# Optimization experiments

Measured on AMD Instinct MI355X. Metric: run time of the kernel, lower is better.

Reference implementation:

```python
import jax, jax.numpy as jnp
import numpy as np

B, C, D, H, W = 4, 128, 16, 16, 16
CQ = C // 8

def setup_inputs() -> dict:
    key = jax.random.key(0)
    ks = jax.random.split(key, 8)
    s = 0.05
    return {
        "x": jax.random.normal(ks[0], (B, C, D, H, W), dtype=jnp.float32),
        "wq": jax.random.normal(ks[1], (CQ, C), dtype=jnp.float32) * s,
        "bq": jax.random.normal(ks[2], (CQ,), dtype=jnp.float32) * s,
        "wk": jax.random.normal(ks[3], (CQ, C), dtype=jnp.float32) * s,
        "bk": jax.random.normal(ks[4], (CQ,), dtype=jnp.float32) * s,
        "wv": jax.random.normal(ks[5], (C, C), dtype=jnp.float32) * s,
        "bv": jax.random.normal(ks[6], (C,), dtype=jnp.float32) * s,
        "gamma": jax.random.normal(ks[7], (1,), dtype=jnp.float32),
    }

def reference(x, wq, bq, wk, bk, wv, bv, gamma):
    b, c, d, h, w = x.shape
    n = d * h * w
    xf = x.reshape(b, c, n)                                  # [B,C,N]
    # 1x1x1 convs == channel-wise linear projections
    q = jnp.einsum('bcn,qc->bqn', xf, wq) + bq[None, :, None]  # [B,CQ,N]
    k = jnp.einsum('bcn,qc->bqn', xf, wk) + bk[None, :, None]  # [B,CQ,N]
    v = jnp.einsum('bcn,oc->bon', xf, wv) + bv[None, :, None]  # [B,C,N]
    # energy[b,i,j] = sum_c q[b,c,i] * k[b,c,j]  (query permuted to [B,N,CQ])
    energy = jnp.einsum('bci,bcj->bij', q, k)                # [B,N,N]
    attn = jax.nn.softmax(energy, axis=-1)                   # [B,N,N]
    # out = bmm(value, attn^T): out[b,c,i] = sum_j v[b,c,j] * attn[b,i,j]
    out = jnp.einsum('bcj,bij->bci', v, attn)                # [B,C,N]
    out = out.reshape(b, c, d, h, w)
    return gamma[0] * out + x
```

## Files before the change

kernel.cpp:

```cpp
#include <hip/hip_runtime.h>
#include <stdint.h>

#define NT 4096
#define L2E 1.44269504f

typedef short s16x8 __attribute__((ext_vector_type(8)));
typedef short s16x4 __attribute__((ext_vector_type(4)));
typedef float f32x16 __attribute__((ext_vector_type(16)));
typedef float f32x4 __attribute__((ext_vector_type(4)));

__device__ __forceinline__ unsigned short f2bf(float f) {
  unsigned int u = __float_as_uint(f);
  u = u + 0x7FFFu + ((u >> 16) & 1u);
  return (unsigned short)(u >> 16);
}

__device__ __forceinline__ void pack_pa(const float* p, s16x8* pa) {
  unsigned w8[8];
#pragma unroll
  for (int m = 0; m < 8; ++m)
    asm("v_cvt_pk_bf16_f32 %0, %1, %2" : "=v"(w8[m]) : "v"(p[2 * m]), "v"(p[2 * m + 1]));
  unsigned a0 = w8[0], b0 = w8[2]; asm("v_permlane32_swap_b32 %0, %1" : "+v"(a0), "+v"(b0));
  unsigned a1 = w8[1], b1 = w8[3]; asm("v_permlane32_swap_b32 %0, %1" : "+v"(a1), "+v"(b1));
  unsigned c0 = w8[4], d0 = w8[6]; asm("v_permlane32_swap_b32 %0, %1" : "+v"(c0), "+v"(d0));
  unsigned c1 = w8[5], d1 = w8[7]; asm("v_permlane32_swap_b32 %0, %1" : "+v"(c1), "+v"(d1));
  union PW { unsigned u[4]; s16x8 v; } q0, q1;
  q0.u[0] = a0; q0.u[1] = a1; q0.u[2] = b0; q0.u[3] = b1;
  q1.u[0] = c0; q1.u[1] = c1; q1.u[2] = d0; q1.u[3] = d1;
  pa[0] = q0.v; pa[1] = q1.v;
}

__device__ __forceinline__ void merge_write(float* scr, const f32x16 (&acc)[4],
                                            int lc, int hi) {
#pragma unroll
  for (int cb = 0; cb < 4; ++cb)
#pragma unroll
    for (int r = 0; r < 16; ++r) {
      int i = (r & 3) + 8 * (r >> 2) + 4 * hi;
      scr[i * 132 + cb * 32 + lc] = acc[cb][r];
    }
}
__device__ __forceinline__ void merge_add(const float* scr, f32x16 (&acc)[4],
                                          int lc, int hi) {
#pragma unroll
  for (int cb = 0; cb < 4; ++cb)
#pragma unroll
    for (int r = 0; r < 16; ++r) {
      int i = (r & 3) + 8 * (r >> 2) + 4 * hi;
      acc[cb][r] += scr[i * 132 + cb * 32 + lc];
    }
}

__global__ __launch_bounds__(512, 2) void proj_kern(
    const float* __restrict__ x,
    const float* __restrict__ wq, const float* __restrict__ bq,
    const float* __restrict__ wk, const float* __restrict__ bk,
    const float* __restrict__ wv, const float* __restrict__ bv,
    short* __restrict__ qws, short* __restrict__ kws, short* __restrict__ vfrag) {
  __shared__ __align__(16) unsigned short w_s[160 * 128];
  __shared__ __align__(16) unsigned short xv_s[128 * 72];

  int t = threadIdx.x;
  int blk = blockIdx.x;
  int b = blk >> 6;
  int n0 = (blk & 63) * 64;

  for (int i4 = t; i4 < 5120; i4 += 512) {
    int row = i4 >> 5, ka = (i4 & 31) * 4;
    f32x4 v;
    float sc = 1.0f;
    if (row < 128)      v = *(const f32x4*)(wv + row * 128 + ka);
    else if (row < 144) v = *(const f32x4*)(wq + (row - 128) * 128 + ka);
    else              { v = *(const f32x4*)(wk + (row - 144) * 128 + ka); sc = L2E; }
    s16x4 o;
#pragma unroll
    for (int j = 0; j < 4; ++j) o[j] = (short)f2bf(v[j] * sc);
    unsigned byt = ((unsigned)(ka * 2)) ^ (((unsigned)row & 7u) << 4);
    *(s16x4*)((char*)w_s + row * 256 + byt) = o;
  }
  {
    int cL = t >> 4, nn4 = (t & 15) * 4;
    for (int cc = 0; cc < 128; cc += 32) {
      int c = cc + cL;
      f32x4 v = *(const f32x4*)(x + ((size_t)b * 128 + c) * NT + n0 + nn4);
      s16x4 o;
#pragma unroll
      for (int j = 0; j < 4; ++j) o[j] = (short)f2bf(v[j]);
      *(s16x4*)(xv_s + c * 64 + nn4) = o;
    }
  }
  __syncthreads();

  int w = t >> 6, lane = t & 63, lc = lane & 31, hi = lane >> 5;
  int rblk = w >> 1, nc = w & 1;
  int nn = nc * 32 + lc;

  f32x16 zf = {0.f,0.f,0.f,0.f,0.f,0.f,0.f,0.f,0.f,0.f,0.f,0.f,0.f,0.f,0.f,0.f};
  f32x16 acc = zf, acc2 = zf;

#pragma unroll
  for (int kk = 0; kk < 8; ++kk) {
    int kb0 = kk * 16 + hi * 8;
    s16x8 xf;
#pragma unroll
    for (int e = 0; e < 8; ++e) xf[e] = (short)xv_s[(kb0 + e) * 64 + nn];
    unsigned byt = ((unsigned)(kk * 32 + hi * 16)) ^ (((unsigned)lc & 7u) << 4);
    s16x8 af = *(const s16x8*)((const char*)w_s + (rblk * 32 + lc) * 256 + byt);
    acc = __builtin_amdgcn_mfma_f32_32x32x16_bf16(af, xf, acc, 0, 0, 0);
    if (rblk == 3) {
      s16x8 af2 = *(const s16x8*)((const char*)w_s + (128 + lc) * 256 + byt);
      acc2 = __builtin_amdgcn_mfma_f32_32x32x16_bf16(af2, xf, acc2, 0, 0, 0);
    }
  }

  if (rblk == 3) {
    size_t nidx = ((size_t)b * NT + n0 + nn) * 16;
    s16x4 q0, q1, k0, k1;
#pragma unroll
    for (int j = 0; j < 4; ++j) {
      q0[j] = (short)f2bf(acc2[j]      + bq[j + 4 * hi]);
      q1[j] = (short)f2bf(acc2[j + 4]  + bq[j + 8 + 4 * hi]);
      k0[j] = (short)f2bf(acc2[j + 8]  + bk[j + 4 * hi] * L2E);
      k1[j] = (short)f2bf(acc2[j + 12] + bk[j + 8 + 4 * hi] * L2E);
    }
    *(s16x4*)(qws + nidx + 4 * hi)     = q0;
    *(s16x4*)(qws + nidx + 8 + 4 * hi) = q1;
    *(s16x4*)(kws + nidx + 4 * hi)     = k0;
    *(s16x4*)(kws + nidx + 8 + 4 * hi) = k1;
  }

  __syncthreads();
#pragma unroll
  for (int r = 0; r < 16; ++r) {
    int c = rblk * 32 + (r & 3) + 8 * (r >> 2) + 4 * hi;
    xv_s[c * 72 + nn] = f2bf(acc[r] + bv[c]);
  }
  __syncthreads();
#pragma unroll
  for (int p = 0; p < 2; ++p) {
    int gid = t + p * 512;
    int c = gid & 127, ng = gid >> 7;
    s16x8 v = *(const s16x8*)(xv_s + c * 72 + ng * 8);
    size_t idx = (((size_t)b * 256 + (n0 >> 4) + (ng >> 1)) * 128 + c) * 16 + (ng & 1) * 8;
    *(s16x8*)(vfrag + idx) = v;
  }
}

__global__ __launch_bounds__(256, 4) void attn_mfma(
    const short* __restrict__ qws, const short* __restrict__ kws, const short* __restrict__ vfrag,
    const float* __restrict__ x, const float* __restrict__ gp, float* __restrict__ out) {
  __shared__ __align__(16) unsigned char lds[34432];

  int g = blockIdx.x;
  int gg = (g & 7) * 64 + (g >> 3);
  int b = gg >> 7;
  int it = gg & 127;
  int t = threadIdx.x;
  int w = t >> 6, lane = t & 63, lc = lane & 31, hi = lane >> 5;
  int jt0 = w * 1024;

  const short* qb = qws + (size_t)b * NT * 16;
  const short* kb = kws + (size_t)b * NT * 16;
  const short* vfb = vfrag + (size_t)b * 256 * 128 * 16;

  s16x8 qf = *(const s16x8*)(qb + (size_t)(it * 32 + lc) * 16 + hi * 8);

  f32x16 zf = {0.f,0.f,0.f,0.f,0.f,0.f,0.f,0.f,0.f,0.f,0.f,0.f,0.f,0.f,0.f,0.f};
  f32x16 acc[4];
#pragma unroll
  for (int j = 0; j < 4; ++j) acc[j] = zf;
  float lsum = 0.f;

  for (int st = 0; st < 32; ++st) {
    int j0 = jt0 + st * 32;
    int jtb = j0 >> 4;
    s16x8 kf = *(const s16x8*)(kb + (size_t)(j0 + lc) * 16 + hi * 8);
    s16x8 v0[4];
#pragma unroll
    for (int cb = 0; cb < 4; ++cb)
      v0[cb] = *(const s16x8*)(vfb + ((size_t)jtb * 128 + cb * 32 + lc) * 16 + hi * 8);

    f32x16 e = __builtin_amdgcn_mfma_f32_32x32x16_bf16(kf, qf, zf, 0, 0, 0);
#pragma unroll
    for (int r = 0; r < 16; ++r) e[r] = __builtin_amdgcn_exp2f(e[r]);
    float a0 = 0.f;
#pragma unroll
    for (int r = 0; r < 16; ++r) a0 += e[r];
    lsum += a0;

    s16x8 pa[2];
    pack_pa((const float*)&e, pa);

    __builtin_amdgcn_s_setprio(1);
#pragma unroll
    for (int cb = 0; cb < 4; ++cb)
      acc[cb] = __builtin_amdgcn_mfma_f32_32x32x16_bf16(pa[0], v0[cb], acc[cb], 0, 0, 0);
    __builtin_amdgcn_s_setprio(0);

    s16x8 v1[4];
#pragma unroll
    for (int cb = 0; cb < 4; ++cb)
      v1[cb] = *(const s16x8*)(vfb + ((size_t)(jtb + 1) * 128 + cb * 32 + lc) * 16 + hi * 8);

    __builtin_amdgcn_s_setprio(1);
#pragma unroll
    for (int cb = 0; cb < 4; ++cb)
      acc[cb] = __builtin_amdgcn_mfma_f32_32x32x16_bf16(pa[1], v1[cb], acc[cb], 0, 0, 0);
    __builtin_amdgcn_s_setprio(0);
  }

  float* rg0  = (float*)lds;
  float* rg1  = (float*)(lds + 16896);
  float* lsc  = (float*)(lds + 33792);
  float* linv = (float*)(lds + 34304);

  float lf = lsum + __shfl_xor(lsum, 32);
  if (hi == 0) lsc[w * 32 + lc] = lf;
  if (w == 2) merge_write(rg0, acc, lc, hi);
  if (w == 3) merge_write(rg1, acc, lc, hi);
  __syncthreads();
  if (t < 32) {
    float L = lsc[t] + lsc[32 + t] + lsc[64 + t] + lsc[96 + t];
    linv[t] = 1.0f / L;
  }
  if (w == 0) merge_add(rg0, acc, lc, hi);
  if (w == 1) merge_add(rg1, acc, lc, hi);
  __syncthreads();
  if (w == 1) merge_write(rg0, acc, lc, hi);
  __syncthreads();
  if (w == 0) {
    merge_add(rg0, acc, lc, hi);
    merge_write(rg0, acc, lc, hi);
  }
  __syncthreads();

  float gam = gp[0];
  int cc = t >> 1, ih = (t & 1) * 16;
  const float* xb = x + ((size_t)b * 128 + cc) * NT + it * 32 + ih;
  float* ob = out + ((size_t)b * 128 + cc) * NT + it * 32 + ih;
#pragma unroll
  for (int q2 = 0; q2 < 4; ++q2) {
    f32x4 xv = *(const f32x4*)(xb + q2 * 4);
    f32x4 ov;
#pragma unroll
    for (int j = 0; j < 4; ++j) {
      int i = ih + q2 * 4 + j;
      ov[j] = gam * rg0[i * 132 + cc] * linv[i] + xv[j];
    }
    *(f32x4*)(ob + q2 * 4) = ov;
  }
}

extern "C" void kernel_launch(void* const* d_in, const int* in_sizes, int n_in,
                              void* d_out, int out_size, void* d_ws, size_t ws_size,
                              hipStream_t stream) {
  const float* x     = (const float*)d_in[0];
  const float* wq    = (const float*)d_in[1];
  const float* bq    = (const float*)d_in[2];
  const float* wk    = (const float*)d_in[3];
  const float* bk    = (const float*)d_in[4];
  const float* wv    = (const float*)d_in[5];
  const float* bv    = (const float*)d_in[6];
  const float* gamma = (const float*)d_in[7];
  float* out = (float*)d_out;

  short* qws   = (short*)d_ws;
  short* kws   = qws + (size_t)4 * NT * 16;
  short* vfrag = kws + (size_t)4 * NT * 16;

  proj_kern<<<256, 512, 0, stream>>>(x, wq, bq, wk, bk, wv, bv, qws, kws, vfrag);
  attn_mfma<<<512, 256, 0, stream>>>(qws, kws, vfrag, x, gamma, out);
}
```

Baseline: 45.05 us.

## Split attention keys across two blocks and merge partials in a separate kernel

Splits the key dimension into two halves, so the attention kernel runs 1024 blocks instead of 512. Each block writes unnormalized partial outputs and row sums to workspace, and a new merge kernel combines them, normalizes, and adds the residual. The inner loop is also software-pipelined: the next QK MFMA and the K fragment two steps ahead are issued during the current step's exp and PV work. This trades extra global traffic (about 16 MB of partials written and read) and one more launch for better occupancy and latency hiding.

```diff
diff --git a/kernel.cpp b/kernel.cpp
--- a/kernel.cpp
+++ b/kernel.cpp
@@ -146,18 +146,19 @@
   }
 }
 
-__global__ __launch_bounds__(256, 4) void attn_mfma(
+__global__ __launch_bounds__(256) void attn_part(
     const short* __restrict__ qws, const short* __restrict__ kws, const short* __restrict__ vfrag,
-    const float* __restrict__ x, const float* __restrict__ gp, float* __restrict__ out) {
+    float* __restrict__ Dp, float* __restrict__ Lp) {
   __shared__ __align__(16) unsigned char lds[34432];
 
   int g = blockIdx.x;
-  int gg = (g & 7) * 64 + (g >> 3);
-  int b = gg >> 7;
-  int it = gg & 127;
+  int gg = (g & 7) * 128 + (g >> 3);
+  int b = gg >> 8;
+  int it = (gg >> 1) & 127;
+  int js = gg & 1;
   int t = threadIdx.x;
   int w = t >> 6, lane = t & 63, lc = lane & 31, hi = lane >> 5;
-  int jt0 = w * 1024;
+  int jt0 = js * 2048 + w * 512;
 
   const short* qb = qws + (size_t)b * NT * 16;
   const short* kb = kws + (size_t)b * NT * 16;
@@ -171,48 +172,52 @@
   for (int j = 0; j < 4; ++j) acc[j] = zf;
   float lsum = 0.f;
 
-  for (int st = 0; st < 32; ++st) {
-    int j0 = jt0 + st * 32;
-    int jtb = j0 >> 4;
-    s16x8 kf = *(const s16x8*)(kb + (size_t)(j0 + lc) * 16 + hi * 8);
-    s16x8 v0[4];
+  s16x8 kfA = *(const s16x8*)(kb + (size_t)(jt0 + lc) * 16 + hi * 8);
+  f32x16 eA = __builtin_amdgcn_mfma_f32_32x32x16_bf16(kfA, qf, zf, 0, 0, 0);
+  s16x8 kfB = *(const s16x8*)(kb + (size_t)(jt0 + 32 + lc) * 16 + hi * 8);
+  f32x16 eB = zf;
+
+  auto body = [&](int st, f32x16& eCur, f32x16& eNxt, s16x8& kfNxt, s16x8& kfFar) {
+    int jtb = (jt0 >> 4) + st * 2;
+    s16x8 vc[2][4];
+#pragma unroll
+    for (int sl = 0; sl < 2; ++sl)
+#pragma unroll
+      for (int cb = 0; cb < 4; ++cb)
+        vc[sl][cb] = *(const s16x8*)(vfb + ((size_t)(jtb + sl) * 128 + cb * 32 + lc) * 16 + hi * 8);
+
+#pragma unroll
+    for (int r = 0; r < 16; ++r) eCur[r] = __builtin_amdgcn_exp2f(eCur[r]);
+    float a0 = 0.f;
+#pragma unroll
+    for (int r = 0; r < 16; ++r) a0 += eCur[r];
+    lsum += a0;
+    s16x8 pa[2];
+    pack_pa((const float*)&eCur, pa);
+
+    if (st < 15)
+      eNxt = __builtin_amdgcn_mfma_f32_32x32x16_bf16(kfNxt, qf, zf, 0, 0, 0);
+    if (st < 14)
+      kfFar = *(const s16x8*)(kb + (size_t)(jt0 + (st + 2) * 32 + lc) * 16 + hi * 8);
+
+    __builtin_amdgcn_s_setprio(1);
 #pragma unroll
     for (int cb = 0; cb < 4; ++cb)
-      v0[cb] = *(const s16x8*)(vfb + ((size_t)jtb * 128 + cb * 32 + lc) * 16 + hi * 8);
-
-    f32x16 e = __builtin_amdgcn_mfma_f32_32x32x16_bf16(kf, qf, zf, 0, 0, 0);
-#pragma unroll
-    for (int r = 0; r < 16; ++r) e[r] = __builtin_amdgcn_exp2f(e[r]);
-    float a0 = 0.f;
-#pragma unroll
-    for (int r = 0; r < 16; ++r) a0 += e[r];
-    lsum += a0;
-
-    s16x8 pa[2];
-    pack_pa((const float*)&e, pa);
-
-    __builtin_amdgcn_s_setprio(1);
+      acc[cb] = __builtin_amdgcn_mfma_f32_32x32x16_bf16(pa[0], vc[0][cb], acc[cb], 0, 0, 0);
 #pragma unroll
     for (int cb = 0; cb < 4; ++cb)
-      acc[cb] = __builtin_amdgcn_mfma_f32_32x32x16_bf16(pa[0], v0[cb], acc[cb], 0, 0, 0);
+      acc[cb] = __builtin_amdgcn_mfma_f32_32x32x16_bf16(pa[1], vc[1][cb], acc[cb], 0, 0, 0);
     __builtin_amdgcn_s_setprio(0);
-
-    s16x8 v1[4];
-#pragma unroll
-    for (int cb = 0; cb < 4; ++cb)
-      v1[cb] = *(const s16x8*)(vfb + ((size_t)(jtb + 1) * 128 + cb * 32 + lc) * 16 + hi * 8);
-
-    __builtin_amdgcn_s_setprio(1);
-#pragma unroll
-    for (int cb = 0; cb < 4; ++cb)
-      acc[cb] = __builtin_amdgcn_mfma_f32_32x32x16_bf16(pa[1], v1[cb], acc[cb], 0, 0, 0);
-    __builtin_amdgcn_s_setprio(0);
-  }
-
-  float* rg0  = (float*)lds;
-  float* rg1  = (float*)(lds + 16896);
-  float* lsc  = (float*)(lds + 33792);
-  float* linv = (float*)(lds + 34304);
+  };
+
+  for (int sp = 0; sp < 8; ++sp) {
+    body(2 * sp,     eA, eB, kfB, kfA);
+    body(2 * sp + 1, eB, eA, kfA, kfB);
+  }
+
+  float* rg0 = (float*)lds;
+  float* rg1 = (float*)(lds + 16896);
+  float* lsc = (float*)(lds + 33792);
 
   float lf = lsum + __shfl_xor(lsum, 32);
   if (hi == 0) lsc[w * 32 + lc] = lf;
@@ -221,34 +226,46 @@
   __syncthreads();
   if (t < 32) {
     float L = lsc[t] + lsc[32 + t] + lsc[64 + t] + lsc[96 + t];
-    linv[t] = 1.0f / L;
+    Lp[((size_t)js * 4 + b) * NT + it * 32 + t] = L;
   }
   if (w == 0) merge_add(rg0, acc, lc, hi);
   if (w == 1) merge_add(rg1, acc, lc, hi);
   __syncthreads();
   if (w == 1) merge_write(rg0, acc, lc, hi);
   __syncthreads();
-  if (w == 0) {
-    merge_add(rg0, acc, lc, hi);
-    merge_write(rg0, acc, lc, hi);
-  }
-  __syncthreads();
-
+  if (w == 0) { merge_add(rg0, acc, lc, hi); merge_write(rg0, acc, lc, hi); }
+  __syncthreads();
+
+  int cc = t >> 1, ih = (t & 1) * 16;
+  float* dp = Dp + (((size_t)js * 4 + b) * 128 + cc) * NT + it * 32 + ih;
+#pragma unroll
+  for (int q2 = 0; q2 < 4; ++q2) {
+    f32x4 ov;
+#pragma unroll
+    for (int j = 0; j < 4; ++j) ov[j] = rg0[(ih + q2 * 4 + j) * 132 + cc];
+    *(f32x4*)(dp + q2 * 4) = ov;
+  }
+}
+
+__global__ __launch_bounds__(256) void merge_kern(
+    const float* __restrict__ Dp, const float* __restrict__ Lp,
+    const float* __restrict__ x, const float* __restrict__ gp,
+    float* __restrict__ out) {
+  int idx = blockIdx.x * 256 + threadIdx.x;
+  size_t off = (size_t)idx * 4;
+  int n = (int)(off & (NT - 1));
+  int b = (int)(off >> 19);
   float gam = gp[0];
-  int cc = t >> 1, ih = (t & 1) * 16;
-  const float* xb = x + ((size_t)b * 128 + cc) * NT + it * 32 + ih;
-  float* ob = out + ((size_t)b * 128 + cc) * NT + it * 32 + ih;
-#pragma unroll
-  for (int q2 = 0; q2 < 4; ++q2) {
-    f32x4 xv = *(const f32x4*)(xb + q2 * 4);
-    f32x4 ov;
-#pragma unroll
-    for (int j = 0; j < 4; ++j) {
-      int i = ih + q2 * 4 + j;
-      ov[j] = gam * rg0[i * 132 + cc] * linv[i] + xv[j];
-    }
-    *(f32x4*)(ob + q2 * 4) = ov;
-  }
+  f32x4 d0 = *(const f32x4*)(Dp + off);
+  f32x4 d1 = *(const f32x4*)(Dp + (size_t)4 * 128 * NT + off);
+  f32x4 l0 = *(const f32x4*)(Lp + (size_t)b * NT + n);
+  f32x4 l1 = *(const f32x4*)(Lp + (size_t)4 * NT + (size_t)b * NT + n);
+  f32x4 xv = *(const f32x4*)(x + off);
+  f32x4 ov;
+#pragma unroll
+  for (int j = 0; j < 4; ++j)
+    ov[j] = gam * (d0[j] + d1[j]) / (l0[j] + l1[j]) + xv[j];
+  *(f32x4*)(out + off) = ov;
 }
 
 extern "C" void kernel_launch(void* const* d_in, const int* in_sizes, int n_in,
@@ -267,7 +284,10 @@
   short* qws   = (short*)d_ws;
   short* kws   = qws + (size_t)4 * NT * 16;
   short* vfrag = kws + (size_t)4 * NT * 16;
+  float* Dp    = (float*)(vfrag + (size_t)4 * 256 * 128 * 16);
+  float* Lp    = Dp + (size_t)2 * 4 * 128 * NT;
 
   proj_kern<<<256, 512, 0, stream>>>(x, wq, bq, wk, bk, wv, bv, qws, kws, vfrag);
-  attn_mfma<<<512, 256, 0, stream>>>(qws, kws, vfrag, x, gamma, out);
-}
+  attn_part<<<1024, 256, 0, stream>>>(qws, kws, vfrag, Dp, Lp);
+  merge_kern<<<2048, 256, 0, stream>>>(Dp, Lp, x, gamma, out);
+}
```

New measurement: 52.97 us. +17.6%, slower.

## Split attention output channels across wave pairs and merge partials with LDS atomics

Applied to the files above, without the earlier changes.

The attention kernel now uses 8 waves per block, with each pair of waves sharing a key segment and splitting the 128 value channels into two halves. Each wave holds half as many accumulators, and the multi-step LDS merge tree is replaced by a single write followed by LDS atomicAdd from the other segments. The aim is lower register pressure and more waves in flight, at the cost of recomputing the QK^T MFMA and exp twice per key tile. LDS atomic contention during the merge is another added cost.

```diff
diff --git a/kernel.cpp b/kernel.cpp
--- a/kernel.cpp
+++ b/kernel.cpp
@@ -30,27 +30,6 @@
   pa[0] = q0.v; pa[1] = q1.v;
 }
 
-__device__ __forceinline__ void merge_write(float* scr, const f32x16 (&acc)[4],
-                                            int lc, int hi) {
-#pragma unroll
-  for (int cb = 0; cb < 4; ++cb)
-#pragma unroll
-    for (int r = 0; r < 16; ++r) {
-      int i = (r & 3) + 8 * (r >> 2) + 4 * hi;
-      scr[i * 132 + cb * 32 + lc] = acc[cb][r];
-    }
-}
-__device__ __forceinline__ void merge_add(const float* scr, f32x16 (&acc)[4],
-                                          int lc, int hi) {
-#pragma unroll
-  for (int cb = 0; cb < 4; ++cb)
-#pragma unroll
-    for (int r = 0; r < 16; ++r) {
-      int i = (r & 3) + 8 * (r >> 2) + 4 * hi;
-      acc[cb][r] += scr[i * 132 + cb * 32 + lc];
-    }
-}
-
 __global__ __launch_bounds__(512, 2) void proj_kern(
     const float* __restrict__ x,
     const float* __restrict__ wq, const float* __restrict__ bq,
@@ -146,10 +125,10 @@
   }
 }
 
-__global__ __launch_bounds__(256, 4) void attn_mfma(
+__global__ __launch_bounds__(512, 4) void attn_mfma(
     const short* __restrict__ qws, const short* __restrict__ kws, const short* __restrict__ vfrag,
     const float* __restrict__ x, const float* __restrict__ gp, float* __restrict__ out) {
-  __shared__ __align__(16) unsigned char lds[34432];
+  __shared__ __align__(16) unsigned char lds[18048];
 
   int g = blockIdx.x;
   int gg = (g & 7) * 64 + (g >> 3);
@@ -157,7 +136,8 @@
   int it = gg & 127;
   int t = threadIdx.x;
   int w = t >> 6, lane = t & 63, lc = lane & 31, hi = lane >> 5;
-  int jt0 = w * 1024;
+  int s = w >> 1, ch = w & 1;
+  int jt0 = s * 1024;
 
   const short* qb = qws + (size_t)b * NT * 16;
   const short* kb = kws + (size_t)b * NT * 16;
@@ -166,19 +146,20 @@
   s16x8 qf = *(const s16x8*)(qb + (size_t)(it * 32 + lc) * 16 + hi * 8);
 
   f32x16 zf = {0.f,0.f,0.f,0.f,0.f,0.f,0.f,0.f,0.f,0.f,0.f,0.f,0.f,0.f,0.f,0.f};
-  f32x16 acc[4];
-#pragma unroll
-  for (int j = 0; j < 4; ++j) acc[j] = zf;
+  f32x16 acc[2];
+  acc[0] = zf; acc[1] = zf;
   float lsum = 0.f;
 
   for (int st = 0; st < 32; ++st) {
     int j0 = jt0 + st * 32;
     int jtb = j0 >> 4;
     s16x8 kf = *(const s16x8*)(kb + (size_t)(j0 + lc) * 16 + hi * 8);
-    s16x8 v0[4];
-#pragma unroll
-    for (int cb = 0; cb < 4; ++cb)
-      v0[cb] = *(const s16x8*)(vfb + ((size_t)jtb * 128 + cb * 32 + lc) * 16 + hi * 8);
+    s16x8 vc[2][2];
+#pragma unroll
+    for (int sl = 0; sl < 2; ++sl)
+#pragma unroll
+      for (int cbi = 0; cbi < 2; ++cbi)
+        vc[sl][cbi] = *(const s16x8*)(vfb + ((size_t)(jtb + sl) * 128 + (ch * 2 + cbi) * 32 + lc) * 16 + hi * 8);
 
     f32x16 e = __builtin_amdgcn_mfma_f32_32x32x16_bf16(kf, qf, zf, 0, 0, 0);
 #pragma unroll
@@ -193,61 +174,60 @@
 
     __builtin_amdgcn_s_setprio(1);
 #pragma unroll
-    for (int cb = 0; cb < 4; ++cb)
-      acc[cb] = __builtin_amdgcn_mfma_f32_32x32x16_bf16(pa[0], v0[cb], acc[cb], 0, 0, 0);
+    for (int sl = 0; sl < 2; ++sl)
+#pragma unroll
+      for (int cbi = 0; cbi < 2; ++cbi)
+        acc[cbi] = __builtin_amdgcn_mfma_f32_32x32x16_bf16(pa[sl], vc[sl][cbi], acc[cbi], 0, 0, 0);
     __builtin_amdgcn_s_setprio(0);
-
-    s16x8 v1[4];
-#pragma unroll
-    for (int cb = 0; cb < 4; ++cb)
-      v1[cb] = *(const s16x8*)(vfb + ((size_t)(jtb + 1) * 128 + cb * 32 + lc) * 16 + hi * 8);
-
-    __builtin_amdgcn_s_setprio(1);
-#pragma unroll
-    for (int cb = 0; cb < 4; ++cb)
-      acc[cb] = __builtin_amdgcn_mfma_f32_32x32x16_bf16(pa[1], v1[cb], acc[cb], 0, 0, 0);
-    __builtin_amdgcn_s_setprio(0);
-  }
-
-  float* rg0  = (float*)lds;
-  float* rg1  = (float*)(lds + 16896);
-  float* lsc  = (float*)(lds + 33792);
-  float* linv = (float*)(lds + 34304);
+  }
+
+  float* rg_my = (float*)(lds + (ch ? 8704 : 0));
+  float* lsc   = (float*)(lds + 17408);
+  float* linv  = (float*)(lds + 17920);
 
   float lf = lsum + __shfl_xor(lsum, 32);
-  if (hi == 0) lsc[w * 32 + lc] = lf;
-  if (w == 2) merge_write(rg0, acc, lc, hi);
-  if (w == 3) merge_write(rg1, acc, lc, hi);
+  if (ch == 0 && hi == 0) lsc[s * 32 + lc] = lf;
+
+  if (s == 0) {
+#pragma unroll
+    for (int cbi = 0; cbi < 2; ++cbi)
+#pragma unroll
+      for (int r = 0; r < 16; ++r) {
+        int i = (r & 3) + 8 * (r >> 2) + 4 * hi;
+        rg_my[i * 68 + cbi * 32 + lc] = acc[cbi][r];
+      }
+  }
   __syncthreads();
   if (t < 32) {
     float L = lsc[t] + lsc[32 + t] + lsc[64 + t] + lsc[96 + t];
     linv[t] = 1.0f / L;
   }
-  if (w == 0) merge_add(rg0, acc, lc, hi);
-  if (w == 1) merge_add(rg1, acc, lc, hi);
-  __syncthreads();
-  if (w == 1) merge_write(rg0, acc, lc, hi);
-  __syncthreads();
-  if (w == 0) {
-    merge_add(rg0, acc, lc, hi);
-    merge_write(rg0, acc, lc, hi);
+  if (s != 0) {
+#pragma unroll
+    for (int cbi = 0; cbi < 2; ++cbi)
+#pragma unroll
+      for (int r = 0; r < 16; ++r) {
+        int i = (r & 3) + 8 * (r >> 2) + 4 * hi;
+        atomicAdd(&rg_my[i * 68 + cbi * 32 + lc], acc[cbi][r]);
+      }
   }
   __syncthreads();
 
   float gam = gp[0];
-  int cc = t >> 1, ih = (t & 1) * 16;
-  const float* xb = x + ((size_t)b * 128 + cc) * NT + it * 32 + ih;
-  float* ob = out + ((size_t)b * 128 + cc) * NT + it * 32 + ih;
-#pragma unroll
-  for (int q2 = 0; q2 < 4; ++q2) {
-    f32x4 xv = *(const f32x4*)(xb + q2 * 4);
+  int cc = t >> 2, iq = t & 3;
+  const float* rgc = (const float*)(lds + ((cc & 64) ? 8704 : 0));
+  int cp = cc & 63;
+  size_t base = ((size_t)b * 128 + cc) * NT + it * 32 + iq * 8;
+#pragma unroll
+  for (int q2 = 0; q2 < 2; ++q2) {
+    f32x4 xv = *(const f32x4*)(x + base + q2 * 4);
     f32x4 ov;
 #pragma unroll
     for (int j = 0; j < 4; ++j) {
-      int i = ih + q2 * 4 + j;
-      ov[j] = gam * rg0[i * 132 + cc] * linv[i] + xv[j];
-    }
-    *(f32x4*)(ob + q2 * 4) = ov;
+      int i = iq * 8 + q2 * 4 + j;
+      ov[j] = gam * rgc[i * 68 + cp] * linv[i] + xv[j];
+    }
+    *(f32x4*)(out + base + q2 * 4) = ov;
   }
 }
 
@@ -269,5 +249,5 @@
   short* vfrag = kws + (size_t)4 * NT * 16;
 
   proj_kern<<<256, 512, 0, stream>>>(x, wq, bq, wk, bk, wv, bv, qws, kws, vfrag);
-  attn_mfma<<<512, 256, 0, stream>>>(qws, kws, vfrag, x, gamma, out);
-}
+  attn_mfma<<<512, 512, 0, stream>>>(qws, kws, vfrag, x, gamma, out);
+}
```

After: 71.46 us. +58.6%, slower.
